# Optimization experiments

Hardware: AMD Instinct MI355X
Metric: run time of the kernel (lower is better)

Reference implementation:

```python
import jax, jax.numpy as jnp
import numpy as np

EPS = 1e-5


def _in_relu(y):
    # instance norm (no affine, biased var, eps=1e-5) + ReLU, y: [B,C,H,W]
    mu = jnp.mean(y, axis=(-2, -1), keepdims=True)
    var = jnp.mean((y - mu) ** 2, axis=(-2, -1), keepdims=True)
    return jax.nn.relu((y - mu) * jax.lax.rsqrt(var + EPS))


def _conv3(x, w, b):
    # x: [C,H,W], w: [O,I,3,3] -> [O,H,W]
    y = jax.lax.conv_general_dilated(x[None], w, (1, 1), ((1, 1), (1, 1)),
                                     dimension_numbers=('NCHW', 'OIHW', 'NCHW'))[0]
    return y + b[:, None, None]


def _mod_block(x, W, b, mod):
    # per-sample weight modulation: mod[n] * W, then conv+IN+relu; x: [B,C,H,W], mod: [B,O,I,3,3]
    y = jax.vmap(lambda xi, mi: _conv3(xi, mi * W, b))(x, mod)
    return _in_relu(y)


def _maxpool2(x):
    return jax.lax.reduce_window(x, -jnp.inf, jax.lax.max, (1, 1, 2, 2), (1, 1, 2, 2), 'VALID')


def _up2(x):
    B, C, H, W = x.shape
    # bilinear, half-pixel centers == PyTorch align_corners=False
    return jax.image.resize(x, (B, C, 2 * H, 2 * W), method='bilinear')


def _conv1x1(x, w, b):
    y = jax.lax.conv_general_dilated(x, w, (1, 1), 'VALID',
                                     dimension_numbers=('NCHW', 'OIHW', 'NCHW'))
    return y + b[None, :, None, None]


def setup_inputs() -> dict:
    key = jax.random.key(0)
    B, H, W = 8, 256, 256
    ks = iter(jax.random.split(key, 64))
    d = {}
    d['us_query_input'] = jax.random.normal(next(ks), (B, 1, H, W), jnp.float32)
    d['ksp_query_imgs'] = jax.random.normal(next(ks), (B, H, W, 2), jnp.float32)
    d['ksp_mask_query'] = jax.random.uniform(next(ks), (B, H, W), jnp.float32)
    down_io = [(1, 32), (32, 64), (64, 128), (128, 256)]
    up_io = [(512, 128), (256, 64), (128, 32), (64, 32)]
    for i, (ci, co) in enumerate(down_io):
        d[f'down_mod_{i}'] = jax.random.normal(next(ks), (B, co, ci, 3, 3), jnp.float32)
        d[f'W_d{i}'] = 0.05 * jax.random.normal(next(ks), (co, ci, 3, 3), jnp.float32)
        d[f'b_d{i}'] = 0.05 * jax.random.normal(next(ks), (co,), jnp.float32)
    d['latent_mod'] = jax.random.normal(next(ks), (B, 256, 256, 3, 3), jnp.float32)
    d['W_lat'] = 0.05 * jax.random.normal(next(ks), (256, 256, 3, 3), jnp.float32)
    d['b_lat'] = 0.05 * jax.random.normal(next(ks), (256,), jnp.float32)
    for i, (ci, co) in enumerate(up_io):
        d[f'up_mod_{i}'] = jax.random.normal(next(ks), (B, co, ci, 3, 3), jnp.float32)
        d[f'W_u{i}'] = 0.05 * jax.random.normal(next(ks), (co, ci, 3, 3), jnp.float32)
        d[f'b_u{i}'] = 0.05 * jax.random.normal(next(ks), (co,), jnp.float32)
    d['w_c1'] = 0.05 * jax.random.normal(next(ks), (16, 32, 1, 1), jnp.float32)
    d['b_c1'] = 0.05 * jax.random.normal(next(ks), (16,), jnp.float32)
    d['w_c2'] = 0.05 * jax.random.normal(next(ks), (1, 16, 1, 1), jnp.float32)
    d['b_c2'] = 0.05 * jax.random.normal(next(ks), (1,), jnp.float32)
    d['w_c3'] = 0.05 * jax.random.normal(next(ks), (1, 1, 1, 1), jnp.float32)
    d['b_c3'] = 0.05 * jax.random.normal(next(ks), (1,), jnp.float32)
    return d


def reference(us_query_input, ksp_query_imgs, ksp_mask_query,
              down_mod_0, down_mod_1, down_mod_2, down_mod_3,
              latent_mod, up_mod_0, up_mod_1, up_mod_2, up_mod_3,
              W_d0, b_d0, W_d1, b_d1, W_d2, b_d2, W_d3, b_d3,
              W_lat, b_lat,
              W_u0, b_u0, W_u1, b_u1, W_u2, b_u2, W_u3, b_u3,
              w_c1, b_c1, w_c2, b_c2, w_c3, b_c3):
    x0 = us_query_input
    out = x0
    skips = []
    downs = [(W_d0, b_d0, down_mod_0), (W_d1, b_d1, down_mod_1),
             (W_d2, b_d2, down_mod_2), (W_d3, b_d3, down_mod_3)]
    for Wc, bc, m in downs:
        out = _mod_block(out, Wc, bc, m)
        skips.append(out)
        out = _maxpool2(out)
    out = _mod_block(out, W_lat, b_lat, latent_mod)
    ups = [(W_u0, b_u0, up_mod_0), (W_u1, b_u1, up_mod_1),
           (W_u2, b_u2, up_mod_2), (W_u3, b_u3, up_mod_3)]
    for Wc, bc, m in ups:
        out = _up2(out)
        out = jnp.concatenate([out, skips.pop()], axis=1)
        out = _mod_block(out, Wc, bc, m)
    out = _conv1x1(_conv1x1(_conv1x1(out, w_c1, b_c1), w_c2, b_c2), w_c3, b_c3)
    out = out + x0
    # FFT data consistency
    pred = out[:, 0]                                  # [B,H,W]
    kpred = jnp.fft.fft2(pred, norm='ortho')
    ksp = ksp_query_imgs[..., 0] + 1j * ksp_query_imgs[..., 1]
    upd = ksp_mask_query * ksp + (1.0 - ksp_mask_query) * kpred
    img = jnp.fft.ifft2(upd, norm='ortho')
    return jnp.real(img)[:, None].astype(jnp.float32)   # [B,1,H,W]
```

## Files before the change

### kernel.cpp

```cpp
#include <hip/hip_runtime.h>


#define EPS_IN 1e-5f

typedef __attribute__((ext_vector_type(8))) short short8;
typedef __attribute__((ext_vector_type(4))) short short4_t;
typedef __attribute__((ext_vector_type(4))) float f32x4;

__device__ __forceinline__ short f2bf(float f) {
    unsigned u = __float_as_uint(f);
    unsigned r = (u + 0x7fffu + ((u >> 16) & 1u)) >> 16;
    return (short)r;
}
__device__ __forceinline__ float bf2f(short s) {
    return __uint_as_float(((unsigned)(unsigned short)s) << 16);
}

__global__ void zero_f(float* __restrict__ p, int n)
{
    int i = blockIdx.x * 256 + threadIdx.x;
    if (i < n) p[i] = 0.f;
}

struct WmJobs {
    const float* W[8];
    const float* mod[8];
    short* wm[8];
    int Co[8];
    int Ci[8];
    int cum[9];
};

__global__ void make_wm_all(WmJobs j)
{
    int idx = blockIdx.x * 256 + threadIdx.x;
    if (idx >= j.cum[8]) return;
    int l = 0;
    while (idx >= j.cum[l + 1]) ++l;
    int local = idx - j.cum[l];
    const int Ci = j.Ci[l], Co = j.Co[l];
    int ci = local % Ci;
    int rem = local / Ci;
    int co = rem % Co;
    int b = rem / Co;
    const float* wp = j.W[l] + (size_t)(co * Ci + ci) * 9;
    const float* mp = j.mod[l] + ((size_t)((size_t)b * Co + co) * Ci + ci) * 9;
    short* wm = j.wm[l];
#pragma unroll
    for (int k = 0; k < 9; ++k)
        wm[(((size_t)(b * 9 + k) * Co + co) * Ci + ci)] = f2bf(wp[k] * mp[k]);
}

template <int VR, int NCOG, bool UP>
__global__ __launch_bounds__(256) void conv3x3_cl(
    const short* __restrict__ x1, int Ci1,
    const short* __restrict__ x2,
    const float2* __restrict__ st1, float invHW1,
    const short* __restrict__ wm,
    short* __restrict__ y,
    float2* __restrict__ stats,
    int Ci, int Co, int H, int W)
{
    constexpr int TH = 4 * VR, SH = TH + 2, SW = 18;
    constexpr int STN = UP ? 256 : 1;
    constexpr bool DW = (TH * 16 * NCOG * 16 * 2) <= (SH * SW * 32 * 2);
    __shared__ __align__(16) short s_x[SH][SW][32];
    __shared__ float s_red[4][4][NCOG][4][2];
    __shared__ float2 s_st1[STN];

    const int tid = threadIdx.x;
    const int lane = tid & 63, wv = tid >> 6;
    const int m = lane & 15, g = lane >> 4;

    const int b = blockIdx.x & 7;
    int r = blockIdx.x >> 3;
    const int nCoB = Co / (16 * NCOG);
    const int coblk = r % nCoB;
    const int tileId = r / nCoB;
    const int tilesx = W >> 4;
    const int tx0 = (tileId % tilesx) * 16;
    const int ty0 = (tileId / tilesx) * TH;
    const int co0 = coblk * (16 * NCOG);
    const int Ci2 = Ci - Ci1;
    const int Hs = H >> 1, Ws = W >> 1;

    if (UP) {
        for (int i = tid; i < Ci1; i += 256) {
            float2 v = st1[(size_t)b * Ci1 + i];
            float mu = v.x * invHW1;
            float var = v.y * invHW1 - mu * mu;
            s_st1[i] = make_float2(mu, rsqrtf(var + EPS_IN));
        }
    }

    f32x4 acc[NCOG][VR];
#pragma unroll
    for (int cg = 0; cg < NCOG; ++cg)
#pragma unroll
        for (int rr = 0; rr < VR; ++rr) acc[cg][rr] = (f32x4)0.f;

    const short* wmb = wm + (size_t)b * 9 * Co * Ci;
    const short* x1b = x1 + (size_t)b * (UP ? (size_t)Hs * Ws : (size_t)H * W) * Ci1;
    const short* x2b = x2 + (size_t)b * H * W * Ci2;

    for (int ci0 = 0; ci0 < Ci; ci0 += 32) {
        __syncthreads();
        if (UP && ci0 < Ci1) {
            const int cb = ci0;
            for (int idx = tid; idx < SH * SW * 4; idx += 256) {
                int gg = idx & 3, pos = idx >> 2;
                int yy = pos / SW, xx = pos - yy * SW;
                int gy = ty0 + yy - 1, gx = tx0 + xx - 1;
                short8 v = (short8)0;
                if (gy >= 0 && gy < H && gx >= 0 && gx < W) {
                    int xk = gx >> 1, yk = gy >> 1;
                    int xo = gx & 1, yo = gy & 1;
                    int xa = xo ? xk : (xk > 0 ? xk - 1 : 0);
                    int xb = xo ? (xk + 1 < Ws ? xk + 1 : Ws - 1) : xk;
                    float wxa = xo ? 0.75f : 0.25f;
                    int ya = yo ? yk : (yk > 0 ? yk - 1 : 0);
                    int yb = yo ? (yk + 1 < Hs ? yk + 1 : Hs - 1) : yk;
                    float wya = yo ? 0.75f : 0.25f;
                    const short* ib = x1b + cb + gg * 8;
                    short8 vaa = *(const short8*)(ib + ((size_t)ya * Ws + xa) * Ci1);
                    short8 vab = *(const short8*)(ib + ((size_t)ya * Ws + xb) * Ci1);
                    short8 vba = *(const short8*)(ib + ((size_t)yb * Ws + xa) * Ci1);
                    short8 vbb = *(const short8*)(ib + ((size_t)yb * Ws + xb) * Ci1);
#pragma unroll
                    for (int e = 0; e < 8; ++e) {
                        float2 sv = s_st1[cb + gg * 8 + e];
                        float aa = fmaxf(0.f, (bf2f(vaa[e]) - sv.x) * sv.y);
                        float ab = fmaxf(0.f, (bf2f(vab[e]) - sv.x) * sv.y);
                        float ba = fmaxf(0.f, (bf2f(vba[e]) - sv.x) * sv.y);
                        float bb = fmaxf(0.f, (bf2f(vbb[e]) - sv.x) * sv.y);
                        float r0 = wxa * aa + (1.f - wxa) * ab;
                        float r1 = wxa * ba + (1.f - wxa) * bb;
                        v[e] = f2bf(wya * r0 + (1.f - wya) * r1);
                    }
                }
                *(short8*)&s_x[yy][xx][(gg ^ (xx & 3)) * 8] = v;
            }
        } else {
            const short* src; int C, cb;
            if (ci0 < Ci1) { src = x1b; C = Ci1; cb = ci0; }
            else           { src = x2b; C = Ci2; cb = ci0 - Ci1; }
            for (int idx = tid; idx < SH * SW * 4; idx += 256) {
                int gg = idx & 3, pos = idx >> 2;
                int yy = pos / SW, xx = pos - yy * SW;
                int gy = ty0 + yy - 1, gx = tx0 + xx - 1;
                short8 v = (short8)0;
                if (gy >= 0 && gy < H && gx >= 0 && gx < W)
                    v = *(const short8*)(src + ((size_t)gy * W + gx) * C + cb + gg * 8);
                *(short8*)&s_x[yy][xx][(gg ^ (xx & 3)) * 8] = v;
            }
        }
        __syncthreads();
#pragma unroll
        for (int t = 0; t < 9; ++t) {
            const int dy = t / 3, dx = t - 3 * (t / 3);
            const short* wr = wmb + ((size_t)t * Co + co0) * Ci + ci0 + g * 8;
            short8 a[NCOG];
#pragma unroll
            for (int cg = 0; cg < NCOG; ++cg)
                a[cg] = *(const short8*)(wr + (size_t)(cg * 16 + m) * Ci);
            const int xx = m + dx;
            const int sgo = (g ^ (xx & 3)) * 8;
#pragma unroll
            for (int rr = 0; rr < VR; ++rr) {
                short8 bf = *(const short8*)&s_x[wv * VR + rr + dy][xx][sgo];
#pragma unroll
                for (int cg = 0; cg < NCOG; ++cg)
                    acc[cg][rr] = __builtin_amdgcn_mfma_f32_16x16x32_bf16(a[cg], bf, acc[cg][rr], 0, 0, 0);
            }
        }
    }

    if constexpr (DW) {
        __syncthreads();
        short* sd = (short*)&s_x[0][0][0];
#pragma unroll
        for (int cg = 0; cg < NCOG; ++cg)
#pragma unroll
            for (int rr = 0; rr < VR; ++rr) {
                short4_t o;
#pragma unroll
                for (int q = 0; q < 4; ++q) o[q] = f2bf(acc[cg][rr][q]);
                *(short4_t*)&sd[((wv * VR + rr) * 16 + m) * (NCOG * 16) + cg * 16 + g * 4] = o;
            }
        __syncthreads();
        constexpr int N16 = TH * 16 * NCOG * 2;
        constexpr int CPR = NCOG * 32;
        for (int c = tid; c < N16; c += 256) {
            int row = c / CPR;
            int o16 = c % CPR;
            int p = o16 / (NCOG * 2);
            int cw = o16 % (NCOG * 2);
            short8 v = *(short8*)&sd[(row * 16 + p) * (NCOG * 16) + cw * 8];
            *(short8*)(y + (((size_t)b * H + ty0 + row) * W + tx0 + p) * Co + co0 + cw * 8) = v;
        }
    } else {
        const int ox = tx0 + m;
#pragma unroll
        for (int cg = 0; cg < NCOG; ++cg)
#pragma unroll
            for (int rr = 0; rr < VR; ++rr) {
                int oy = ty0 + wv * VR + rr;
                short4_t o;
#pragma unroll
                for (int q = 0; q < 4; ++q) o[q] = f2bf(acc[cg][rr][q]);
                *(short4_t*)(y + (((size_t)b * H + oy) * W + ox) * Co + co0 + cg * 16 + g * 4) = o;
            }
    }

#pragma unroll
    for (int cg = 0; cg < NCOG; ++cg)
#pragma unroll
        for (int q = 0; q < 4; ++q) {
            float s = 0.f, s2 = 0.f;
#pragma unroll
            for (int rr = 0; rr < VR; ++rr) { float v = acc[cg][rr][q]; s += v; s2 += v * v; }
#pragma unroll
            for (int msk = 1; msk < 16; msk <<= 1) { s += __shfl_xor(s, msk); s2 += __shfl_xor(s2, msk); }
            if (m == 0) { s_red[wv][g][cg][q][0] = s; s_red[wv][g][cg][q][1] = s2; }
        }
    __syncthreads();
    for (int i = tid; i < 16 * NCOG; i += 256) {
        int q = i & 3, gg = (i >> 2) & 3, cg = i >> 4;
        float S = 0.f, S2 = 0.f;
#pragma unroll
        for (int w = 0; w < 4; ++w) { S += s_red[w][gg][cg][q][0]; S2 += s_red[w][gg][cg][q][1]; }
        float* sp = (float*)&stats[(size_t)b * Co + co0 + i];
        atomicAdd(sp, S); atomicAdd(sp + 1, S2);
    }
}

__global__ __launch_bounds__(256) void conv_d0_cl(
    const float* __restrict__ x0, const float* __restrict__ W,
    const float* __restrict__ mod, short* __restrict__ y,
    float2* __restrict__ stats)
{
    __shared__ float s[18][18];
    __shared__ float sw[32][9];
    __shared__ float s_red[4][32][2];
    __shared__ __align__(16) short sd[16][16][32];
    const int tid = threadIdx.x;
    const int tx = tid & 15, ty = tid >> 4;
    const int tx0 = (blockIdx.x & 15) * 16, ty0 = (blockIdx.x >> 4) * 16;
    const int b = blockIdx.y;
    if (tid < 288) sw[tid / 9][tid % 9] = W[tid] * mod[b * 288 + tid];
    for (int pos = tid; pos < 18 * 18; pos += 256) {
        int yy = pos / 18, xx = pos - yy * 18;
        int gy = ty0 + yy - 1, gx = tx0 + xx - 1;
        bool inb = gy >= 0 && gy < 256 && gx >= 0 && gx < 256;
        s[yy][xx] = inb ? x0[((size_t)b << 16) + gy * 256 + gx] : 0.f;
    }
    __syncthreads();
    float v[3][3];
#pragma unroll
    for (int r = 0; r < 3; ++r)
#pragma unroll
        for (int c = 0; c < 3; ++c) v[r][c] = s[ty + r][tx + c];
    float vals[32];
#pragma unroll
    for (int co = 0; co < 32; ++co) {
        float a = 0.f;
#pragma unroll
        for (int r = 0; r < 3; ++r)
#pragma unroll
            for (int c = 0; c < 3; ++c) a = fmaf(v[r][c], sw[co][r * 3 + c], a);
        vals[co] = a;
    }
#pragma unroll
    for (int j = 0; j < 4; ++j) {
        short8 o;
#pragma unroll
        for (int e = 0; e < 8; ++e) o[e] = f2bf(vals[j * 8 + e]);
        *(short8*)&sd[ty][tx][j * 8] = o;
    }
    const int lane = tid & 63, wv = tid >> 6;
#pragma unroll
    for (int co = 0; co < 32; ++co) {
        float sm = vals[co], s2 = vals[co] * vals[co];
#pragma unroll
        for (int off = 32; off > 0; off >>= 1) { sm += __shfl_down(sm, off); s2 += __shfl_down(s2, off); }
        if (lane == 0) { s_red[wv][co][0] = sm; s_red[wv][co][1] = s2; }
    }
    __syncthreads();
    for (int c = tid; c < 1024; c += 256) {
        int row = c >> 6, o = c & 63;
        short8 vv = *(short8*)&sd[row][o >> 2][(o & 3) * 8];
        *(short8*)(y + (((size_t)b * 256 + ty0 + row) * 256 + tx0 + (o >> 2)) * 32 + (o & 3) * 8) = vv;
    }
    if (tid < 32) {
        float S = 0.f, S2 = 0.f;
#pragma unroll
        for (int w = 0; w < 4; ++w) { S += s_red[w][tid][0]; S2 += s_red[w][tid][1]; }
        float* sp = (float*)&stats[(size_t)b * 32 + tid];
        atomicAdd(sp, S); atomicAdd(sp + 1, S2);
    }
}

__global__ void maxpool_cl(short* __restrict__ in,
                           const float2* __restrict__ st, float invHW,
                           short* __restrict__ out,
                           int c8s, int ws, int hs, int total8)
{
    const int C = 8 << c8s;
    for (int idx = blockIdx.x * 256 + threadIdx.x; idx < total8; idx += gridDim.x * 256) {
        int c8 = idx & ((1 << c8s) - 1);
        int p = idx >> c8s;
        int x = p & ((1 << ws) - 1);
        int yy = (p >> ws) & ((1 << hs) - 1);
        int b = p >> (ws + hs);
        short* ip = in + (((size_t)b * (2 << hs) + 2 * yy) * (2 << ws) + 2 * x) * C + c8 * 8;
        size_t rs = (size_t)(2 << ws) * C;
        short8 v0 = *(const short8*)ip, v1 = *(const short8*)(ip + C);
        short8 v2 = *(const short8*)(ip + rs), v3 = *(const short8*)(ip + rs + C);
        short8 o, w0, w1, w2, w3;
#pragma unroll
        for (int e = 0; e < 8; ++e) {
            float2 sv = st[(size_t)b * C + c8 * 8 + e];
            float mu = sv.x * invHW;
            float rsig = rsqrtf(sv.y * invHW - mu * mu + EPS_IN);
            float n0 = fmaxf(0.f, (bf2f(v0[e]) - mu) * rsig);
            float n1 = fmaxf(0.f, (bf2f(v1[e]) - mu) * rsig);
            float n2 = fmaxf(0.f, (bf2f(v2[e]) - mu) * rsig);
            float n3 = fmaxf(0.f, (bf2f(v3[e]) - mu) * rsig);
            w0[e] = f2bf(n0); w1[e] = f2bf(n1); w2[e] = f2bf(n2); w3[e] = f2bf(n3);
            o[e] = f2bf(fmaxf(fmaxf(n0, n1), fmaxf(n2, n3)));
        }
        *(short8*)ip = w0;
        *(short8*)(ip + C) = w1;
        *(short8*)(ip + rs) = w2;
        *(short8*)(ip + rs + C) = w3;
        *(short8*)(out + (size_t)idx * 8) = o;
    }
}

__global__ void upsample_cl(const short* __restrict__ in,
                            const float2* __restrict__ st, float invHW,
                            short* __restrict__ out,
                            int c8s, int wsi, int hsi, int total8)
{
    const int C = 8 << c8s;
    const int Win = 1 << wsi, Hin = 1 << hsi;
    for (int idx = blockIdx.x * 256 + threadIdx.x; idx < total8; idx += gridDim.x * 256) {
        int c8 = idx & ((1 << c8s) - 1);
        int p = idx >> c8s;
        int x = p & (2 * Win - 1);
        int yy = (p >> (wsi + 1)) & (2 * Hin - 1);
        int b = p >> (wsi + 1 + hsi + 1);
        int xk = x >> 1, yk = yy >> 1;
        int xa, xb; float wxa;
        if (x & 1) { xa = xk; xb = (xk + 1 < Win) ? xk + 1 : Win - 1; wxa = 0.75f; }
        else       { xa = (xk > 0) ? xk - 1 : 0; xb = xk; wxa = 0.25f; }
        int ya, yb; float wya;
        if (yy & 1) { ya = yk; yb = (yk + 1 < Hin) ? yk + 1 : Hin - 1; wya = 0.75f; }
        else        { ya = (yk > 0) ? yk - 1 : 0; yb = yk; wya = 0.25f; }
        const short* ib = in + (size_t)b * Hin * Win * C + c8 * 8;
        short8 vaa = *(const short8*)(ib + ((size_t)ya * Win + xa) * C);
        short8 vab = *(const short8*)(ib + ((size_t)ya * Win + xb) * C);
        short8 vba = *(const short8*)(ib + ((size_t)yb * Win + xa) * C);
        short8 vbb = *(const short8*)(ib + ((size_t)yb * Win + xb) * C);
        short8 o;
#pragma unroll
        for (int e = 0; e < 8; ++e) {
            float2 sv = st[(size_t)b * C + c8 * 8 + e];
            float mu = sv.x * invHW;
            float rsig = rsqrtf(sv.y * invHW - mu * mu + EPS_IN);
            float aa = fmaxf(0.f, (bf2f(vaa[e]) - mu) * rsig);
            float ab = fmaxf(0.f, (bf2f(vab[e]) - mu) * rsig);
            float ba = fmaxf(0.f, (bf2f(vba[e]) - mu) * rsig);
            float bb = fmaxf(0.f, (bf2f(vbb[e]) - mu) * rsig);
            float r0 = wxa * aa + (1.f - wxa) * ab;
            float r1 = wxa * ba + (1.f - wxa) * bb;
            o[e] = f2bf(wya * r0 + (1.f - wya) * r1);
        }
        *(short8*)(out + (size_t)idx * 8) = o;
    }
}

__global__ void eff1x1(const float* __restrict__ w1, const float* __restrict__ b1,
                       const float* __restrict__ w2, const float* __restrict__ b2,
                       const float* __restrict__ w3, const float* __restrict__ b3,
                       float* __restrict__ eff)
{
    int t = threadIdx.x;
    if (t < 32) {
        float s = 0.f;
        for (int k = 0; k < 16; ++k) s += w2[k] * w1[k * 32 + t];
        eff[t] = w3[0] * s;
    }
    if (t == 32) {
        float s = 0.f;
        for (int k = 0; k < 16; ++k) s += w2[k] * b1[k];
        eff[32] = w3[0] * (s + b2[0]) + b3[0];
    }
}

__device__ __forceinline__ void fft256(float2* s, int tid, float sign)
{
    __syncthreads();
#pragma unroll
    for (int t = 0; t < 4; ++t) {
        int i = tid + t * 64;
        int r = __brev(i) >> 24;
        if (r > i) { float2 tmp = s[i]; s[i] = s[r]; s[r] = tmp; }
    }
    __syncthreads();
    for (int st = 1; st <= 8; ++st) {
        int m = 1 << st, half = m >> 1;
#pragma unroll
        for (int t = 0; t < 2; ++t) {
            int k = tid + t * 64;
            int g = k >> (st - 1), j = k & (half - 1);
            int i0 = (g << st) + j, i1 = i0 + half;
            float ang = sign * 6.283185307179586f * (float)j / (float)m;
            float sn, cs;
            __sincosf(ang, &sn, &cs);
            float2 a = s[i0], b = s[i1];
            float2 tt = make_float2(b.x * cs - b.y * sn, b.x * sn + b.y * cs);
            s[i0] = make_float2(a.x + tt.x, a.y + tt.y);
            s[i1] = make_float2(a.x - tt.x, a.y - tt.y);
        }
        __syncthreads();
    }
}

__global__ __launch_bounds__(64) void final_fft_rows(
    const short* __restrict__ act, const float2* __restrict__ st, float invHW,
    const float* __restrict__ x0, const float* __restrict__ eff,
    float2* __restrict__ cplx)
{
    __shared__ float2 s[256];
    __shared__ float2 sst[32];
    __shared__ float seff[33];
    const int row = blockIdx.x, tid = threadIdx.x;
    const int b = row >> 8, yy = row & 255;
    if (tid < 32) {
        float2 v = st[(size_t)b * 32 + tid];
        float mu = v.x * invHW;
        sst[tid] = make_float2(mu, rsqrtf(v.y * invHW - mu * mu + EPS_IN));
    }
    if (tid < 33) seff[tid] = eff[tid];
    __syncthreads();
#pragma unroll
    for (int k = 0; k < 4; ++k) {
        int x = k * 64 + tid;
        const short8* a = (const short8*)(act + (((size_t)b * 256 + yy) * 256 + x) * 32);
        float sacc = seff[32] + x0[((size_t)b << 16) + (yy << 8) + x];
#pragma unroll
        for (int j = 0; j < 4; ++j) {
            short8 v = a[j];
#pragma unroll
            for (int e = 0; e < 8; ++e) {
                float2 sv = sst[j * 8 + e];
                sacc += seff[j * 8 + e] * fmaxf(0.f, (bf2f(v[e]) - sv.x) * sv.y);
            }
        }
        s[x] = make_float2(sacc, 0.f);
    }
    fft256(s, tid, -1.f);
    float2* o = cplx + (size_t)row * 256;
    for (int i = tid; i < 256; i += 64) o[i] = s[i];
}

__global__ __launch_bounds__(64) void fft_cols_combine(float2* __restrict__ data,
                                                       const float* __restrict__ ksp,
                                                       const float* __restrict__ mask)
{
    __shared__ float2 s[256];
    int col = blockIdx.x & 255, b = blockIdx.x >> 8;
    int tid = threadIdx.x;
    float2* base = data + (size_t)b * 65536 + col;
    for (int i = tid; i < 256; i += 64) s[i] = base[(size_t)i * 256];
    fft256(s, tid, -1.f);
    for (int i = tid; i < 256; i += 64) {
        size_t mi = ((size_t)b * 256 + i) * 256 + col;
        float m = mask[mi];
        float2 kp = s[i];
        float kr = ksp[mi * 2], ki = ksp[mi * 2 + 1];
        s[i] = make_float2(m * kr + (1.f - m) * kp.x * (1.f / 256.f),
                           m * ki + (1.f - m) * kp.y * (1.f / 256.f));
    }
    fft256(s, tid, 1.f);
    for (int i = tid; i < 256; i += 64) base[(size_t)i * 256] = s[i];
}

__global__ __launch_bounds__(64) void fft_rows_inv(const float2* __restrict__ data,
                                                   float* __restrict__ out)
{
    __shared__ float2 s[256];
    int row = blockIdx.x, tid = threadIdx.x;
    const float2* p = data + (size_t)row * 256;
    for (int i = tid; i < 256; i += 64) s[i] = p[i];
    fft256(s, tid, 1.f);
    float* o = out + (size_t)row * 256;
    for (int i = tid; i < 256; i += 64) o[i] = s[i].x * (1.f / 256.f);
}

extern "C" void kernel_launch(void* const* d_in, const int* in_sizes, int n_in,
                              void* d_out, int out_size, void* d_ws, size_t ws_size,
                              hipStream_t stream)
{
    (void)in_sizes; (void)n_in; (void)out_size; (void)ws_size;

    const float* x0 = (const float*)d_in[0];
    const float* ksp = (const float*)d_in[1];
    const float* mask = (const float*)d_in[2];
    const float* mod_d[4] = {(const float*)d_in[3], (const float*)d_in[6],
                             (const float*)d_in[9], (const float*)d_in[12]};
    const float* W_d[4] = {(const float*)d_in[4], (const float*)d_in[7],
                           (const float*)d_in[10], (const float*)d_in[13]};
    const float* mod_lat = (const float*)d_in[15];
    const float* W_lat = (const float*)d_in[16];
    const float* mod_u[4] = {(const float*)d_in[18], (const float*)d_in[21],
                             (const float*)d_in[24], (const float*)d_in[27]};
    const float* W_u[4] = {(const float*)d_in[19], (const float*)d_in[22],
                           (const float*)d_in[25], (const float*)d_in[28]};
    const float* w_c1 = (const float*)d_in[30];
    const float* b_c1 = (const float*)d_in[31];
    const float* w_c2 = (const float*)d_in[32];
    const float* b_c2 = (const float*)d_in[33];
    const float* w_c3 = (const float*)d_in[34];
    const float* b_c3 = (const float*)d_in[35];

    short* sA  = (short*)d_ws;
    short* sB  = sA + 16777216;
    short* sk0 = sB + 16777216;
    short* sk1 = sk0 + 16777216;
    short* sk2 = sk1 + 8388608;
    short* sk3 = sk2 + 4194304;
    short* wm_d1 = sk3 + 2097152;
    short* wm_d2 = wm_d1 + 147456;
    short* wm_d3 = wm_d2 + 589824;
    short* wm_lat = wm_d3 + 2359296;
    short* wm_u0 = wm_lat + 4718592;
    short* wm_u1 = wm_u0 + 4718592;
    short* wm_u2 = wm_u1 + 1179648;
    short* wm_u3 = wm_u2 + 294912;
    float2* cplx = (float2*)(wm_u3 + 147456);
    float2* stA = cplx + 524288;
    float* eff = (float*)(stA + 7936);

    float2* st_d0 = stA + 0;
    float2* st_d1 = stA + 256;
    float2* st_d2 = stA + 768;
    float2* st_d3 = stA + 1792;
    float2* st_lat = stA + 3840;
    float2* st_u0 = stA + 5888;
    float2* st_u1 = stA + 6912;
    float2* st_u2 = stA + 7424;
    float2* st_u3 = stA + 7680;

    const float i64k = 1.f / 65536.f, i16k = 1.f / 16384.f, i4k = 1.f / 4096.f,
                i1k = 1.f / 1024.f, i256 = 1.f / 256.f;

    dim3 blk(256);

    zero_f<<<62, blk, 0, stream>>>((float*)stA, 15872);
    eff1x1<<<1, 64, 0, stream>>>(w_c1, b_c1, w_c2, b_c2, w_c3, b_c3, eff);

    WmJobs jobs;
    const float* Wl[8]  = {W_d[1], W_d[2], W_d[3], W_lat, W_u[0], W_u[1], W_u[2], W_u[3]};
    const float* Ml[8]  = {mod_d[1], mod_d[2], mod_d[3], mod_lat, mod_u[0], mod_u[1], mod_u[2], mod_u[3]};
    short* WMl[8] = {wm_d1, wm_d2, wm_d3, wm_lat, wm_u0, wm_u1, wm_u2, wm_u3};
    int Col[8] = {64, 128, 256, 256, 128, 64, 32, 32};
    int Cil[8] = {32, 64, 128, 256, 512, 256, 128, 64};
    jobs.cum[0] = 0;
    for (int l = 0; l < 8; ++l) {
        jobs.W[l] = Wl[l]; jobs.mod[l] = Ml[l]; jobs.wm[l] = WMl[l];
        jobs.Co[l] = Col[l]; jobs.Ci[l] = Cil[l];
        jobs.cum[l + 1] = jobs.cum[l] + 8 * Col[l] * Cil[l];
    }
    make_wm_all<<<(jobs.cum[8] + 255) / 256, blk, 0, stream>>>(jobs);

    conv_d0_cl<<<dim3(256, 8), blk, 0, stream>>>(x0, W_d[0], mod_d[0], sk0, st_d0);
    maxpool_cl<<<2048, blk, 0, stream>>>(sk0, st_d0, i64k, sA, 2, 7, 7, 524288);

    conv3x3_cl<4, 4, false><<<512, blk, 0, stream>>>(sA, 32, sA, stA, 0.f, wm_d1, sk1, st_d1, 32, 64, 128, 128);
    maxpool_cl<<<1024, blk, 0, stream>>>(sk1, st_d1, i16k, sA, 3, 6, 6, 262144);

    conv3x3_cl<2, 4, false><<<512, blk, 0, stream>>>(sA, 64, sA, stA, 0.f, wm_d2, sk2, st_d2, 64, 128, 64, 64);
    maxpool_cl<<<512, blk, 0, stream>>>(sk2, st_d2, i4k, sA, 4, 5, 5, 131072);

    conv3x3_cl<2, 2, false><<<512, blk, 0, stream>>>(sA, 128, sA, stA, 0.f, wm_d3, sk3, st_d3, 128, 256, 32, 32);
    maxpool_cl<<<256, blk, 0, stream>>>(sk3, st_d3, i1k, sA, 5, 4, 4, 65536);

    conv3x3_cl<2, 1, false><<<256, blk, 0, stream>>>(sA, 256, sA, stA, 0.f, wm_lat, sB, st_lat, 256, 256, 16, 16);

    upsample_cl<<<1024, blk, 0, stream>>>(sB, st_lat, i256, sA, 5, 4, 4, 262144);
    conv3x3_cl<2, 1, false><<<512, blk, 0, stream>>>(sA, 256, sk3, stA, 0.f, wm_u0, sB, st_u0, 512, 128, 32, 32);
    conv3x3_cl<2, 2, true><<<512, blk, 0, stream>>>(sB, 128, sk2, st_u0, i1k, wm_u1, sA, st_u1, 256, 64, 64, 64);
    conv3x3_cl<4, 2, true><<<512, blk, 0, stream>>>(sA, 64, sk1, st_u1, i4k, wm_u2, sB, st_u2, 128, 32, 128, 128);
    conv3x3_cl<4, 2, true><<<2048, blk, 0, stream>>>(sB, 32, sk0, st_u2, i16k, wm_u3, sA, st_u3, 64, 32, 256, 256);

    final_fft_rows<<<2048, 64, 0, stream>>>(sA, st_u3, i64k, x0, eff, cplx);

    fft_cols_combine<<<2048, 64, 0, stream>>>(cplx, ksp, mask);
    fft_rows_inv<<<2048, 64, 0, stream>>>(cplx, (float*)d_out);
}
```

Baseline: 496.1 us.

## Spread instance-norm stat atomics over eight buckets and cache stats in LDS

Instance-norm sum/sumsq atomics are now spread over 8 replicated buckets chosen by tile index, which reduces contention on the same addresses. Consumers (maxpool, upsample, conv UP prologue, final FFT) sum the 8 buckets. Maxpool and upsample precompute mu/rsigma per (batch, channel) into shared memory once per block instead of doing a global load and rsqrt per element. conv_d0 replaces 32 per-channel wave shuffle reductions with a column sum over the bf16 tile in LDS. In exchange every consumer block re-reads 8x the stats, the zeroed region grows, and conv_d0 stats now come from bf16-rounded values.

New measurement: 471.3 us. 1.05x faster.

```diff
diff --git a/kernel.cpp b/kernel.cpp
--- a/kernel.cpp
+++ b/kernel.cpp
@@ -2,6 +2,7 @@
 
 
 #define EPS_IN 1e-5f
+constexpr int STST = 7936;
 
 typedef __attribute__((ext_vector_type(8))) short short8;
 typedef __attribute__((ext_vector_type(4))) short short4_t;
@@ -83,12 +84,18 @@
     const int co0 = coblk * (16 * NCOG);
     const int Ci2 = Ci - Ci1;
     const int Hs = H >> 1, Ws = W >> 1;
+    const int bucket = tileId & 7;
 
     if (UP) {
         for (int i = tid; i < Ci1; i += 256) {
-            float2 v = st1[(size_t)b * Ci1 + i];
-            float mu = v.x * invHW1;
-            float var = v.y * invHW1 - mu * mu;
+            float sx = 0.f, sy = 0.f;
+#pragma unroll
+            for (int k = 0; k < 8; ++k) {
+                float2 v = st1[(size_t)k * STST + (size_t)b * Ci1 + i];
+                sx += v.x; sy += v.y;
+            }
+            float mu = sx * invHW1;
+            float var = sy * invHW1 - mu * mu;
             s_st1[i] = make_float2(mu, rsqrtf(var + EPS_IN));
         }
     }
@@ -229,7 +236,7 @@
         float S = 0.f, S2 = 0.f;
 #pragma unroll
         for (int w = 0; w < 4; ++w) { S += s_red[w][gg][cg][q][0]; S2 += s_red[w][gg][cg][q][1]; }
-        float* sp = (float*)&stats[(size_t)b * Co + co0 + i];
+        float* sp = (float*)&stats[(size_t)bucket * STST + (size_t)b * Co + co0 + i];
         atomicAdd(sp, S); atomicAdd(sp + 1, S2);
     }
 }
@@ -241,7 +248,7 @@
 {
     __shared__ float s[18][18];
     __shared__ float sw[32][9];
-    __shared__ float s_red[4][32][2];
+    __shared__ float s_red[8][32][2];
     __shared__ __align__(16) short sd[16][16][32];
     const int tid = threadIdx.x;
     const int tx = tid & 15, ty = tid >> 4;
@@ -277,35 +284,53 @@
         for (int e = 0; e < 8; ++e) o[e] = f2bf(vals[j * 8 + e]);
         *(short8*)&sd[ty][tx][j * 8] = o;
     }
-    const int lane = tid & 63, wv = tid >> 6;
-#pragma unroll
-    for (int co = 0; co < 32; ++co) {
-        float sm = vals[co], s2 = vals[co] * vals[co];
-#pragma unroll
-        for (int off = 32; off > 0; off >>= 1) { sm += __shfl_down(sm, off); s2 += __shfl_down(s2, off); }
-        if (lane == 0) { s_red[wv][co][0] = sm; s_red[wv][co][1] = s2; }
-    }
     __syncthreads();
     for (int c = tid; c < 1024; c += 256) {
         int row = c >> 6, o = c & 63;
         short8 vv = *(short8*)&sd[row][o >> 2][(o & 3) * 8];
         *(short8*)(y + (((size_t)b * 256 + ty0 + row) * 256 + tx0 + (o >> 2)) * 32 + (o & 3) * 8) = vv;
     }
+    {
+        const int c = tid & 31, grp = tid >> 5;
+        const short* sdf = (const short*)sd;
+        float ss = 0.f, ss2 = 0.f;
+#pragma unroll
+        for (int p = 0; p < 32; ++p) {
+            float vv = bf2f(sdf[(grp * 32 + p) * 32 + c]);
+            ss += vv; ss2 += vv * vv;
+        }
+        s_red[grp][c][0] = ss;
+        s_red[grp][c][1] = ss2;
+    }
+    __syncthreads();
     if (tid < 32) {
         float S = 0.f, S2 = 0.f;
 #pragma unroll
-        for (int w = 0; w < 4; ++w) { S += s_red[w][tid][0]; S2 += s_red[w][tid][1]; }
-        float* sp = (float*)&stats[(size_t)b * 32 + tid];
+        for (int g2 = 0; g2 < 8; ++g2) { S += s_red[g2][tid][0]; S2 += s_red[g2][tid][1]; }
+        int bucket = blockIdx.x & 7;
+        float* sp = (float*)&stats[(size_t)bucket * STST + (size_t)b * 32 + tid];
         atomicAdd(sp, S); atomicAdd(sp + 1, S2);
     }
 }
 
-__global__ void maxpool_cl(short* __restrict__ in,
-                           const float2* __restrict__ st, float invHW,
-                           short* __restrict__ out,
-                           int c8s, int ws, int hs, int total8)
+__global__ __launch_bounds__(256) void maxpool_cl(
+    short* __restrict__ in, const float2* __restrict__ st, float invHW,
+    short* __restrict__ out, int c8s, int ws, int hs, int total8)
 {
     const int C = 8 << c8s;
+    __shared__ float2 sst[2048];
+    for (int i = threadIdx.x; i < 8 * C; i += 256) {
+        int bb = i / C, c = i % C;
+        float sx = 0.f, sy = 0.f;
+#pragma unroll
+        for (int k = 0; k < 8; ++k) {
+            float2 v = st[(size_t)k * STST + (size_t)bb * C + c];
+            sx += v.x; sy += v.y;
+        }
+        float mu = sx * invHW;
+        sst[i] = make_float2(mu, rsqrtf(sy * invHW - mu * mu + EPS_IN));
+    }
+    __syncthreads();
     for (int idx = blockIdx.x * 256 + threadIdx.x; idx < total8; idx += gridDim.x * 256) {
         int c8 = idx & ((1 << c8s) - 1);
         int p = idx >> c8s;
@@ -319,13 +344,11 @@
         short8 o, w0, w1, w2, w3;
 #pragma unroll
         for (int e = 0; e < 8; ++e) {
-            float2 sv = st[(size_t)b * C + c8 * 8 + e];
-            float mu = sv.x * invHW;
-            float rsig = rsqrtf(sv.y * invHW - mu * mu + EPS_IN);
-            float n0 = fmaxf(0.f, (bf2f(v0[e]) - mu) * rsig);
-            float n1 = fmaxf(0.f, (bf2f(v1[e]) - mu) * rsig);
-            float n2 = fmaxf(0.f, (bf2f(v2[e]) - mu) * rsig);
-            float n3 = fmaxf(0.f, (bf2f(v3[e]) - mu) * rsig);
+            float2 sv = sst[b * C + c8 * 8 + e];
+            float n0 = fmaxf(0.f, (bf2f(v0[e]) - sv.x) * sv.y);
+            float n1 = fmaxf(0.f, (bf2f(v1[e]) - sv.x) * sv.y);
+            float n2 = fmaxf(0.f, (bf2f(v2[e]) - sv.x) * sv.y);
+            float n3 = fmaxf(0.f, (bf2f(v3[e]) - sv.x) * sv.y);
             w0[e] = f2bf(n0); w1[e] = f2bf(n1); w2[e] = f2bf(n2); w3[e] = f2bf(n3);
             o[e] = f2bf(fmaxf(fmaxf(n0, n1), fmaxf(n2, n3)));
         }
@@ -337,13 +360,25 @@
     }
 }
 
-__global__ void upsample_cl(const short* __restrict__ in,
-                            const float2* __restrict__ st, float invHW,
-                            short* __restrict__ out,
-                            int c8s, int wsi, int hsi, int total8)
+__global__ __launch_bounds__(256) void upsample_cl(
+    const short* __restrict__ in, const float2* __restrict__ st, float invHW,
+    short* __restrict__ out, int c8s, int wsi, int hsi, int total8)
 {
     const int C = 8 << c8s;
     const int Win = 1 << wsi, Hin = 1 << hsi;
+    __shared__ float2 sst[2048];
+    for (int i = threadIdx.x; i < 8 * C; i += 256) {
+        int bb = i / C, c = i % C;
+        float sx = 0.f, sy = 0.f;
+#pragma unroll
+        for (int k = 0; k < 8; ++k) {
+            float2 v = st[(size_t)k * STST + (size_t)bb * C + c];
+            sx += v.x; sy += v.y;
+        }
+        float mu = sx * invHW;
+        sst[i] = make_float2(mu, rsqrtf(sy * invHW - mu * mu + EPS_IN));
+    }
+    __syncthreads();
     for (int idx = blockIdx.x * 256 + threadIdx.x; idx < total8; idx += gridDim.x * 256) {
         int c8 = idx & ((1 << c8s) - 1);
         int p = idx >> c8s;
@@ -365,13 +400,11 @@
         short8 o;
 #pragma unroll
         for (int e = 0; e < 8; ++e) {
-            float2 sv = st[(size_t)b * C + c8 * 8 + e];
-            float mu = sv.x * invHW;
-            float rsig = rsqrtf(sv.y * invHW - mu * mu + EPS_IN);
-            float aa = fmaxf(0.f, (bf2f(vaa[e]) - mu) * rsig);
-            float ab = fmaxf(0.f, (bf2f(vab[e]) - mu) * rsig);
-            float ba = fmaxf(0.f, (bf2f(vba[e]) - mu) * rsig);
-            float bb = fmaxf(0.f, (bf2f(vbb[e]) - mu) * rsig);
+            float2 sv = sst[b * C + c8 * 8 + e];
+            float aa = fmaxf(0.f, (bf2f(vaa[e]) - sv.x) * sv.y);
+            float ab = fmaxf(0.f, (bf2f(vab[e]) - sv.x) * sv.y);
+            float ba = fmaxf(0.f, (bf2f(vba[e]) - sv.x) * sv.y);
+            float bb = fmaxf(0.f, (bf2f(vbb[e]) - sv.x) * sv.y);
             float r0 = wxa * aa + (1.f - wxa) * ab;
             float r1 = wxa * ba + (1.f - wxa) * bb;
             o[e] = f2bf(wya * r0 + (1.f - wya) * r1);
@@ -438,9 +471,14 @@
     const int row = blockIdx.x, tid = threadIdx.x;
     const int b = row >> 8, yy = row & 255;
     if (tid < 32) {
-        float2 v = st[(size_t)b * 32 + tid];
-        float mu = v.x * invHW;
-        sst[tid] = make_float2(mu, rsqrtf(v.y * invHW - mu * mu + EPS_IN));
+        float sx = 0.f, sy = 0.f;
+#pragma unroll
+        for (int k = 0; k < 8; ++k) {
+            float2 v = st[(size_t)k * STST + (size_t)b * 32 + tid];
+            sx += v.x; sy += v.y;
+        }
+        float mu = sx * invHW;
+        sst[tid] = make_float2(mu, rsqrtf(sy * invHW - mu * mu + EPS_IN));
     }
     if (tid < 33) seff[tid] = eff[tid];
     __syncthreads();
@@ -541,7 +579,7 @@
     short* wm_u3 = wm_u2 + 294912;
     float2* cplx = (float2*)(wm_u3 + 147456);
     float2* stA = cplx + 524288;
-    float* eff = (float*)(stA + 7936);
+    float* eff = (float*)(stA + 8 * STST);
 
     float2* st_d0 = stA + 0;
     float2* st_d1 = stA + 256;
@@ -558,7 +596,7 @@
 
     dim3 blk(256);
 
-    zero_f<<<62, blk, 0, stream>>>((float*)stA, 15872);
+    zero_f<<<496, blk, 0, stream>>>((float*)stA, 8 * STST * 2);
     eff1x1<<<1, 64, 0, stream>>>(w_c1, b_c1, w_c2, b_c2, w_c3, b_c3, eff);
 
     WmJobs jobs;
```
